# Kernel optimization log

Measured on AMD Instinct MI355X. Metric: run time of the kernel, lower is better.

The kernel has to match this reference:

```python
import jax, jax.numpy as jnp
import numpy as np

DIMS = 1024
STATE = 2 * DIMS
EPS = 1e-8


def _rmsnorm(v, scale):
    # norm = ||v||_2 * d^{-1/2}
    d = v.shape[-1]
    n = jnp.sqrt(jnp.sum(v * v, axis=-1, keepdims=True)) * (d ** -0.5)
    return scale * v / (n + EPS)


def setup_inputs() -> dict:
    key = jax.random.key(0)
    ks = jax.random.split(key, 5)
    x = jax.random.normal(ks[0], (4, 2048, DIMS), dtype=jnp.float32)
    ls_scale = jnp.ones((DIMS // 2,), dtype=jnp.float32)
    rs_scale = jnp.ones((DIMS // 2,), dtype=jnp.float32)
    split_scale = jnp.full((DIMS,), 0.1, dtype=jnp.float32)
    sk = (1.0 / DIMS) ** 0.5
    Wk = jax.random.uniform(ks[1], (DIMS, STATE), jnp.float32, -sk, sk)
    Wugg = jax.random.uniform(ks[2], (DIMS, 3 * STATE), jnp.float32, -sk, sk)
    so = (1.0 / STATE) ** 0.5
    Wout = jax.random.uniform(ks[3], (STATE, DIMS), jnp.float32, -so, so)
    return {"x": x, "ls_scale": ls_scale, "rs_scale": rs_scale,
            "split_scale": split_scale, "Wk": Wk, "Wugg": Wugg, "Wout": Wout}


def reference(x, ls_scale, rs_scale, split_scale, Wk, Wugg, Wout):
    residual = x
    # RMS_split norm (output_dim=None)
    xl, xr = jnp.split(x, 2, axis=-1)
    xn = jnp.concatenate([_rmsnorm(xl, ls_scale), _rmsnorm(xr, rs_scale)], axis=-1)
    xn = xn * split_scale

    K = jax.nn.sigmoid(xn @ Wk)                      # [B,S,STATE]
    u, g_in, g_out = jnp.split(xn @ Wugg, 3, axis=-1)
    u = u * jax.nn.sigmoid(g_in) * (1.0 - K)

    # linear recurrence: h_0 = u_0; h_t = K_{t-1} * h_{t-1} + u_t
    a = jnp.concatenate([jnp.ones_like(K[..., :1, :]), K[..., :-1, :]], axis=-2)

    def combine(lhs, rhs):
        aL, bL = lhs
        aR, bR = rhs
        return (aL * aR, bL * aR + bR)

    _, h = jax.lax.associative_scan(combine, (a, u), axis=1)
    outputs = h * jax.nn.sigmoid(g_out)
    y = outputs @ Wout
    return y + residual
```

## Files before the change

### kernel.cpp

```cpp
#include <hip/hip_runtime.h>
#include <hip/hip_bf16.h>
#include <stdint.h>

#define DIMS 1024
#define STATE 2048
#define BATCH 4
#define SEQ 2048
#define TOKENS 8192
#define N1 8192
#define NCHUNK 16
#define CHUNKL (SEQ / NCHUNK)

typedef __hip_bfloat16 bf16;
typedef __attribute__((ext_vector_type(8))) short bf16x8;
typedef __attribute__((ext_vector_type(4))) float f32x4;
typedef __attribute__((ext_vector_type(16))) float f32x16;

__device__ __forceinline__ float sigmoidf_(float x) {
  return 1.0f / (1.0f + __expf(-x));
}

__device__ __forceinline__ void async_copy16(const void* g, void* l) {
  __builtin_amdgcn_global_load_lds(
      (const __attribute__((address_space(1))) void*)(uintptr_t)g,
      (__attribute__((address_space(3))) void*)(uint32_t)(uintptr_t)l,
      16, 0, 0);
}

__device__ __forceinline__ int swz32(int row, int kc) {
  int line = row >> 1;
  int sub = ((row & 1) << 2) | kc;
  return (line << 3) | (sub ^ (line & 7));
}
__device__ __forceinline__ void swz32_dec(int c, int& row, int& kc) {
  int line = c >> 3;
  int sub = (c & 7) ^ (line & 7);
  row = (line << 1) | (sub >> 2);
  kc = sub & 3;
}
__device__ __forceinline__ int swz64(int row, int kc) {
  return (row << 3) | (kc ^ (row & 7));
}
__device__ __forceinline__ void swz64_dec(int c, int& row, int& kc) {
  row = c >> 3;
  kc = (c & 7) ^ (row & 7);
}

__global__ __launch_bounds__(256) void transpose_bf16_kernel(
    const float* __restrict__ W, bf16* __restrict__ Wt, int K, int N) {
  __shared__ float tile[32][33];
  int tx = threadIdx.x & 31;
  int ty = threadIdx.x >> 5;
  long col = (long)blockIdx.x * 32 + tx;
  long rowb = (long)blockIdx.y * 32;
#pragma unroll
  for (int i = 0; i < 32; i += 8)
    tile[ty + i][tx] = W[(rowb + ty + i) * N + col];
  __syncthreads();
  long ocol = rowb + tx;
  long orow = (long)blockIdx.x * 32 + ty;
#pragma unroll
  for (int i = 0; i < 32; i += 8)
    Wt[(orow + i) * K + ocol] = __float2bfloat16(tile[tx][ty + i]);
}

__global__ __launch_bounds__(256) void rmsnorm_kernel(
    const float* __restrict__ x, const float* __restrict__ ls,
    const float* __restrict__ rs, const float* __restrict__ ss,
    bf16* __restrict__ xn) {
  int token = blockIdx.x;
  int tid = threadIdx.x;
  const float4* xt = (const float4*)(x + (long)token * DIMS);
  float4 v = xt[tid];
  float s = v.x * v.x + v.y * v.y + v.z * v.z + v.w * v.w;
#pragma unroll
  for (int d = 32; d > 0; d >>= 1) s += __shfl_down(s, d);
  __shared__ float parts[4];
  if ((tid & 63) == 0) parts[tid >> 6] = s;
  __syncthreads();
  int j = tid * 4;
  bool left = j < 512;
  float sum = left ? (parts[0] + parts[1]) : (parts[2] + parts[3]);
  float n = sqrtf(sum * (1.0f / 512.0f));
  float inv = 1.0f / (n + 1e-8f);
  const float4* sc = (const float4*)(left ? ls : rs);
  float4 g = sc[left ? tid : tid - 128];
  float4 p = ((const float4*)ss)[tid];
  bf16* o = xn + (long)token * DIMS + j;
  o[0] = __float2bfloat16(v.x * g.x * inv * p.x);
  o[1] = __float2bfloat16(v.y * g.y * inv * p.y);
  o[2] = __float2bfloat16(v.z * g.z * inv * p.z);
  o[3] = __float2bfloat16(v.w * g.w * inv * p.w);
}

__device__ __forceinline__ void g1_stage(const bf16* __restrict__ A,
                                         const bf16* __restrict__ Bt,
                                         long arow0, long brow0, int k0,
                                         int wave, int lane, bf16* As, bf16* Bs) {
  const int K = DIMS;
#pragma unroll
  for (int i = 0; i < 4; i++) {
    int c = (wave * 4 + i) * 64 + lane;
    int row, kc; swz32_dec(c, row, kc);
    async_copy16(A + (arow0 + row) * K + k0 + kc * 8, (char*)As + (wave * 4 + i) * 1024);
  }
#pragma unroll
  for (int i = 0; i < 2; i++) {
    int c = (wave * 2 + i) * 64 + lane;
    int row, kc; swz32_dec(c, row, kc);
    async_copy16(Bt + (brow0 + row) * K + k0 + kc * 8, (char*)Bs + (wave * 2 + i) * 1024);
  }
}

__global__ __launch_bounds__(256, 2) void gemm1_big(
    const bf16* __restrict__ A, const bf16* __restrict__ Bt, bf16* __restrict__ C) {
  __shared__ __align__(16) bf16 As0[256 * 32], As1[256 * 32];
  __shared__ __align__(16) bf16 Bs0[128 * 32], Bs1[128 * 32];
  int tid = threadIdx.x;
  int lane = tid & 63, wave = tid >> 6;
  int wm = wave & 1, wn = wave >> 1;
  long arow0 = (long)blockIdx.y * 256;
  long brow0 = (long)blockIdx.x * 128;
  int m_lane = lane & 31, q4 = lane >> 5;
  f32x16 acc[4][2] = {};

  g1_stage(A, Bt, arow0, brow0, 0, wave, lane, As0, Bs0);
  __syncthreads();

  for (int it = 0; it < 32; it += 2) {
    {
      const bf16x8* AsV = (const bf16x8*)As0;
      const bf16x8* BsV = (const bf16x8*)Bs0;
      bf16x8 af[2][4], bfr[2][2];
#pragma unroll
      for (int ks = 0; ks < 2; ks++) {
        int kc = ks * 2 + q4;
#pragma unroll
        for (int mt = 0; mt < 4; mt++) af[ks][mt] = AsV[swz32(wm * 128 + mt * 32 + m_lane, kc)];
#pragma unroll
        for (int nt = 0; nt < 2; nt++) bfr[ks][nt] = BsV[swz32(wn * 64 + nt * 32 + m_lane, kc)];
      }
      g1_stage(A, Bt, arow0, brow0, (it + 1) * 32, wave, lane, As1, Bs1);
#pragma unroll
      for (int ks = 0; ks < 2; ks++)
#pragma unroll
        for (int mt = 0; mt < 4; mt++)
#pragma unroll
          for (int nt = 0; nt < 2; nt++)
            acc[mt][nt] = __builtin_amdgcn_mfma_f32_32x32x16_bf16(bfr[ks][nt], af[ks][mt], acc[mt][nt], 0, 0, 0);
      __syncthreads();
    }
    {
      const bf16x8* AsV = (const bf16x8*)As1;
      const bf16x8* BsV = (const bf16x8*)Bs1;
      bf16x8 af[2][4], bfr[2][2];
#pragma unroll
      for (int ks = 0; ks < 2; ks++) {
        int kc = ks * 2 + q4;
#pragma unroll
        for (int mt = 0; mt < 4; mt++) af[ks][mt] = AsV[swz32(wm * 128 + mt * 32 + m_lane, kc)];
#pragma unroll
        for (int nt = 0; nt < 2; nt++) bfr[ks][nt] = BsV[swz32(wn * 64 + nt * 32 + m_lane, kc)];
      }
      if (it + 2 < 32)
        g1_stage(A, Bt, arow0, brow0, (it + 2) * 32, wave, lane, As0, Bs0);
#pragma unroll
      for (int ks = 0; ks < 2; ks++)
#pragma unroll
        for (int mt = 0; mt < 4; mt++)
#pragma unroll
          for (int nt = 0; nt < 2; nt++)
            acc[mt][nt] = __builtin_amdgcn_mfma_f32_32x32x16_bf16(bfr[ks][nt], af[ks][mt], acc[mt][nt], 0, 0, 0);
      __syncthreads();
    }
  }
#pragma unroll
  for (int mt = 0; mt < 4; mt++) {
    long row = arow0 + wm * 128 + mt * 32 + m_lane;
#pragma unroll
    for (int nt = 0; nt < 2; nt++) {
#pragma unroll
      for (int g = 0; g < 4; g++) {
        long col = brow0 + wn * 64 + nt * 32 + g * 8 + q4 * 4;
        bf16 tmp[4];
#pragma unroll
        for (int j = 0; j < 4; j++) tmp[j] = __float2bfloat16(acc[mt][nt][g * 4 + j]);
        *(uint2*)(C + row * N1 + col) = *(uint2*)tmp;
      }
    }
  }
}

__device__ __forceinline__ void g2_stage(const bf16* __restrict__ A,
                                         const bf16* __restrict__ Bt,
                                         long arow0, long brow0, int k0, int K,
                                         int wave, int lane, bf16* As, bf16* Bs) {
#pragma unroll
  for (int i = 0; i < 4; i++) {
    int c = (wave * 4 + i) * 64 + lane;
    int row, kc; swz64_dec(c, row, kc);
    async_copy16(A + (arow0 + row) * K + k0 + kc * 8, (char*)As + (wave * 4 + i) * 1024);
    async_copy16(Bt + (brow0 + row) * K + k0 + kc * 8, (char*)Bs + (wave * 4 + i) * 1024);
  }
}

__global__ __launch_bounds__(256) void gemm2_resid(
    const bf16* __restrict__ A, const bf16* __restrict__ Bt,
    float* __restrict__ C, const float* __restrict__ resid) {
  __shared__ __align__(16) bf16 As0[128 * 64], As1[128 * 64];
  __shared__ __align__(16) bf16 Bs0[128 * 64], Bs1[128 * 64];
  const int K = STATE, N = DIMS;
  int tid = threadIdx.x;
  int lane = tid & 63, wave = tid >> 6;
  int wm = wave & 1, wn = wave >> 1;
  long arow0 = (long)blockIdx.y * 128;
  long brow0 = (long)blockIdx.x * 128;
  int r = lane & 15, q = lane >> 4;
  f32x4 acc[4][4] = {};

  g2_stage(A, Bt, arow0, brow0, 0, K, wave, lane, As0, Bs0);
  __syncthreads();

  for (int it = 0; it < 32; it += 2) {
    {
      const bf16x8* AsV = (const bf16x8*)As0;
      const bf16x8* BsV = (const bf16x8*)Bs0;
      bf16x8 af[2][4], bfr[2][4];
#pragma unroll
      for (int ks = 0; ks < 2; ks++) {
#pragma unroll
        for (int mt = 0; mt < 4; mt++) af[ks][mt] = AsV[swz64(wm * 64 + mt * 16 + r, ks * 4 + q)];
#pragma unroll
        for (int nt = 0; nt < 4; nt++) bfr[ks][nt] = BsV[swz64(wn * 64 + nt * 16 + r, ks * 4 + q)];
      }
      g2_stage(A, Bt, arow0, brow0, (it + 1) * 64, K, wave, lane, As1, Bs1);
#pragma unroll
      for (int ks = 0; ks < 2; ks++)
#pragma unroll
        for (int mt = 0; mt < 4; mt++)
#pragma unroll
          for (int nt = 0; nt < 4; nt++)
            acc[mt][nt] = __builtin_amdgcn_mfma_f32_16x16x32_bf16(bfr[ks][nt], af[ks][mt], acc[mt][nt], 0, 0, 0);
      __syncthreads();
    }
    {
      const bf16x8* AsV = (const bf16x8*)As1;
      const bf16x8* BsV = (const bf16x8*)Bs1;
      bf16x8 af[2][4], bfr[2][4];
#pragma unroll
      for (int ks = 0; ks < 2; ks++) {
#pragma unroll
        for (int mt = 0; mt < 4; mt++) af[ks][mt] = AsV[swz64(wm * 64 + mt * 16 + r, ks * 4 + q)];
#pragma unroll
        for (int nt = 0; nt < 4; nt++) bfr[ks][nt] = BsV[swz64(wn * 64 + nt * 16 + r, ks * 4 + q)];
      }
      if (it + 2 < 32)
        g2_stage(A, Bt, arow0, brow0, (it + 2) * 64, K, wave, lane, As0, Bs0);
#pragma unroll
      for (int ks = 0; ks < 2; ks++)
#pragma unroll
        for (int mt = 0; mt < 4; mt++)
#pragma unroll
          for (int nt = 0; nt < 4; nt++)
            acc[mt][nt] = __builtin_amdgcn_mfma_f32_16x16x32_bf16(bfr[ks][nt], af[ks][mt], acc[mt][nt], 0, 0, 0);
      __syncthreads();
    }
  }

#pragma unroll
  for (int mt = 0; mt < 4; mt++) {
    long row = arow0 + wm * 64 + mt * 16 + r;
#pragma unroll
    for (int nt = 0; nt < 4; nt++) {
      long col = brow0 + wn * 64 + nt * 16 + q * 4;
      float4 rv = *(const float4*)(resid + row * N + col);
      float4 ov;
      ov.x = acc[mt][nt][0] + rv.x;
      ov.y = acc[mt][nt][1] + rv.y;
      ov.z = acc[mt][nt][2] + rv.z;
      ov.w = acc[mt][nt][3] + rv.w;
      *(float4*)(C + row * N + col) = ov;
    }
  }
}


__global__ __launch_bounds__(256) void chunk_summary_kernel(
    const bf16* __restrict__ C1, float* __restrict__ carryA,
    float* __restrict__ carryU) {
  int b = blockIdx.x;
  int ch = blockIdx.y * 256 + threadIdx.x;
  int chunk = blockIdx.z;
  int t0 = chunk * CHUNKL;
  long base = ((long)b * SEQ) * N1 + ch;
  float kp = 0.0f;
  if (chunk != 0) kp = __bfloat162float(C1[base + (long)(t0 - 1) * N1]);
  float a_first = (chunk == 0) ? 1.0f : sigmoidf_(kp);
  float A = 1.0f, U = 0.0f;
#pragma unroll 8
  for (int t = t0; t < t0 + CHUNKL; t++) {
    long off = base + (long)t * N1;
    float kraw = __bfloat162float(C1[off]);
    float uraw = __bfloat162float(C1[off + 2048]);
    float gin  = __bfloat162float(C1[off + 4096]);
    float a = (t == t0) ? a_first : sigmoidf_(kp);
    float sK = sigmoidf_(kraw);
    float u = uraw * sigmoidf_(gin) * (1.0f - sK);
    A *= a;
    U = a * U + u;
    kp = kraw;
  }
  int cidx = (b * NCHUNK + chunk) * STATE + ch;
  carryA[cidx] = A;
  carryU[cidx] = U;
}

__global__ __launch_bounds__(256) void carry_scan_kernel(
    const float* __restrict__ carryA, const float* __restrict__ carryU,
    float* __restrict__ carryIn) {
  int idx = blockIdx.x * 256 + threadIdx.x;
  int b = idx >> 11;
  int ch = idx & 2047;
  float h = 0.0f;
#pragma unroll
  for (int c = 0; c < NCHUNK; c++) {
    int cidx = (b * NCHUNK + c) * STATE + ch;
    carryIn[cidx] = h;
    h = carryA[cidx] * h + carryU[cidx];
  }
}

__global__ __launch_bounds__(256) void scan_chunk_kernel(
    const bf16* __restrict__ C1, const float* __restrict__ carryIn,
    bf16* __restrict__ out) {
  int b = blockIdx.x;
  int c0 = blockIdx.y * 32;
  int chunk = blockIdx.z;
  int tstart = chunk * CHUNKL;
  __shared__ float a_s[32][65], u_s[32][65], h_s[32][65];
  int tid = threadIdx.x;
  int lane = tid & 63, wave = tid >> 6;
  int cc = tid & 31;
  int tq = tid >> 5;

  float carryH[8], carryK[8];
#pragma unroll
  for (int i = 0; i < 8; i++) {
    int ch = c0 + wave * 8 + i;
    carryH[i] = carryIn[(b * NCHUNK + chunk) * STATE + ch];
    carryK[i] = (chunk == 0)
                    ? 1.0f
                    : sigmoidf_(__bfloat162float(
                          C1[((long)(b * SEQ + tstart - 1)) * N1 + ch]));
  }

  float g_r[8];
  for (int t0 = tstart; t0 < tstart + CHUNKL; t0 += 64) {
#pragma unroll
    for (int i = 0; i < 8; i++) {
      int t = tq * 8 + i;
      long rowoff = ((long)(b * SEQ + t0 + t)) * N1 + c0 + cc;
      float kraw = __bfloat162float(C1[rowoff]);
      float uraw = __bfloat162float(C1[rowoff + 2048]);
      float gin  = __bfloat162float(C1[rowoff + 4096]);
      float gout = __bfloat162float(C1[rowoff + 6144]);
      float aK = sigmoidf_(kraw);
      a_s[cc][t] = aK;
      u_s[cc][t] = uraw * sigmoidf_(gin) * (1.0f - aK);
      g_r[i] = sigmoidf_(gout);
    }
    __syncthreads();
#pragma unroll
    for (int i = 0; i < 8; i++) {
      int ch = wave * 8 + i;
      float aK = a_s[ch][lane];
      float u = u_s[ch][lane];
      float a = __shfl_up(aK, 1);
      if (lane == 0) a = carryK[i];
      float A = a, U = u;
#pragma unroll
      for (int d = 1; d < 64; d <<= 1) {
        float Au = __shfl_up(A, d);
        float Uu = __shfl_up(U, d);
        if (lane >= d) { U += A * Uu; A *= Au; }
      }
      float h = U + A * carryH[i];
      carryH[i] = __shfl(h, 63);
      carryK[i] = __shfl(aK, 63);
      h_s[ch][lane] = h;
    }
    __syncthreads();
#pragma unroll
    for (int i = 0; i < 8; i++) {
      int t = tq * 8 + i;
      out[((long)(b * SEQ + t0 + t)) * STATE + c0 + cc] =
          __float2bfloat16(h_s[cc][t] * g_r[i]);
    }
    __syncthreads();
  }
}

extern "C" void kernel_launch(void* const* d_in, const int* in_sizes, int n_in,
                              void* d_out, int out_size, void* d_ws, size_t ws_size,
                              hipStream_t stream) {
  const float* x    = (const float*)d_in[0];
  const float* ls   = (const float*)d_in[1];
  const float* rs   = (const float*)d_in[2];
  const float* ss   = (const float*)d_in[3];
  const float* Wk   = (const float*)d_in[4];
  const float* Wugg = (const float*)d_in[5];
  const float* Wout = (const float*)d_in[6];
  float* out = (float*)d_out;

  char* ws = (char*)d_ws;
  bf16* W1t = (bf16*)ws;
  bf16* W2t = (bf16*)(ws + 16777216);
  bf16* xn  = (bf16*)(ws + 16777216 + 4194304);
  bf16* C1  = (bf16*)(ws + 16777216 + 4194304 + 16777216);
  bf16* sco = (bf16*)(ws + 16777216 + 4194304 + 16777216 + 134217728);
  float* carryA  = (float*)xn;
  float* carryU  = carryA + BATCH * NCHUNK * STATE;
  float* carryIn = carryU + BATCH * NCHUNK * STATE;

  transpose_bf16_kernel<<<dim3(STATE / 32, DIMS / 32), 256, 0, stream>>>(Wk, W1t, DIMS, STATE);
  transpose_bf16_kernel<<<dim3(3 * STATE / 32, DIMS / 32), 256, 0, stream>>>(
      Wugg, W1t + (long)STATE * DIMS, DIMS, 3 * STATE);
  transpose_bf16_kernel<<<dim3(DIMS / 32, STATE / 32), 256, 0, stream>>>(Wout, W2t, STATE, DIMS);

  rmsnorm_kernel<<<TOKENS, 256, 0, stream>>>(x, ls, rs, ss, xn);

  gemm1_big<<<dim3(N1 / 128, TOKENS / 256), 256, 0, stream>>>(xn, W1t, C1);

  chunk_summary_kernel<<<dim3(BATCH, STATE / 256, NCHUNK), 256, 0, stream>>>(
      C1, carryA, carryU);
  carry_scan_kernel<<<dim3(BATCH * STATE / 256), 256, 0, stream>>>(
      carryA, carryU, carryIn);
  scan_chunk_kernel<<<dim3(BATCH, STATE / 32, NCHUNK), 256, 0, stream>>>(
      C1, carryIn, sco);

  gemm2_resid<<<dim3(DIMS / 128, TOKENS / 128), 256, 0, stream>>>(
      sco, W2t, out, x);
}
```

Baseline: 444.8 us.

## Run the first projection GEMM in FP8 with static scaling

Quantizes the normalized activations and the Wk/Wugg weights to FP8 e4m3 with fixed power-of-two scales, and runs the first large GEMM with FP8 MFMA instructions. The K dimension is permuted so that each 16-byte LDS load feeds two MFMAs. The goal is to halve the memory traffic and LDS footprint per K step and to use the higher FP8 matrix throughput. The cost is lower precision in the gate and input projections, which may not meet the accuracy tolerance.

After: 404.8 us. 1.1x faster.

```diff
diff --git a/kernel.cpp b/kernel.cpp
--- a/kernel.cpp
+++ b/kernel.cpp
@@ -1,5 +1,6 @@
 #include <hip/hip_runtime.h>
 #include <hip/hip_bf16.h>
+#include <hip/hip_fp8.h>
 #include <stdint.h>
 
 #define DIMS 1024
@@ -12,12 +13,27 @@
 #define CHUNKL (SEQ / NCHUNK)
 
 typedef __hip_bfloat16 bf16;
+typedef unsigned char u8;
 typedef __attribute__((ext_vector_type(8))) short bf16x8;
 typedef __attribute__((ext_vector_type(4))) float f32x4;
 typedef __attribute__((ext_vector_type(16))) float f32x16;
+typedef __attribute__((ext_vector_type(2))) long v2i64;
+
+#define XN_SCALE 32.0f
+#define W1_SCALE 256.0f
+#define INV_SCALE (1.0f / 8192.0f)
 
 __device__ __forceinline__ float sigmoidf_(float x) {
   return 1.0f / (1.0f + __expf(-x));
+}
+
+__device__ __forceinline__ u8 to_fp8(float f) {
+  __hip_fp8_e4m3 h(f);
+  return h.__x;
+}
+
+__device__ __forceinline__ int kperm(int k) {
+  return (k & ~24) | ((k & 8) << 1) | ((k & 16) >> 1);
 }
 
 __device__ __forceinline__ void async_copy16(const void* g, void* l) {
@@ -64,10 +80,28 @@
     Wt[(orow + i) * K + ocol] = __float2bfloat16(tile[tx][ty + i]);
 }
 
+__global__ __launch_bounds__(256) void transpose_fp8_kernel(
+    const float* __restrict__ W, u8* __restrict__ Wt, int K, int N) {
+  __shared__ float tile[32][33];
+  int tx = threadIdx.x & 31;
+  int ty = threadIdx.x >> 5;
+  long col = (long)blockIdx.x * 32 + tx;
+  long rowb = (long)blockIdx.y * 32;
+#pragma unroll
+  for (int i = 0; i < 32; i += 8)
+    tile[ty + i][tx] = W[(rowb + ty + i) * N + col];
+  __syncthreads();
+  long ocol = rowb + kperm(tx);
+  long orow = (long)blockIdx.x * 32 + ty;
+#pragma unroll
+  for (int i = 0; i < 32; i += 8)
+    Wt[(orow + i) * K + ocol] = to_fp8(tile[tx][ty + i] * W1_SCALE);
+}
+
 __global__ __launch_bounds__(256) void rmsnorm_kernel(
     const float* __restrict__ x, const float* __restrict__ ls,
     const float* __restrict__ rs, const float* __restrict__ ss,
-    bf16* __restrict__ xn) {
+    u8* __restrict__ xn8) {
   int token = blockIdx.x;
   int tid = threadIdx.x;
   const float4* xt = (const float4*)(x + (long)token * DIMS);
@@ -86,36 +120,37 @@
   const float4* sc = (const float4*)(left ? ls : rs);
   float4 g = sc[left ? tid : tid - 128];
   float4 p = ((const float4*)ss)[tid];
-  bf16* o = xn + (long)token * DIMS + j;
-  o[0] = __float2bfloat16(v.x * g.x * inv * p.x);
-  o[1] = __float2bfloat16(v.y * g.y * inv * p.y);
-  o[2] = __float2bfloat16(v.z * g.z * inv * p.z);
-  o[3] = __float2bfloat16(v.w * g.w * inv * p.w);
-}
-
-__device__ __forceinline__ void g1_stage(const bf16* __restrict__ A,
-                                         const bf16* __restrict__ Bt,
-                                         long arow0, long brow0, int k0,
-                                         int wave, int lane, bf16* As, bf16* Bs) {
+  u8 q[4];
+  q[0] = to_fp8(v.x * g.x * inv * p.x * XN_SCALE);
+  q[1] = to_fp8(v.y * g.y * inv * p.y * XN_SCALE);
+  q[2] = to_fp8(v.z * g.z * inv * p.z * XN_SCALE);
+  q[3] = to_fp8(v.w * g.w * inv * p.w * XN_SCALE);
+  *(uint32_t*)(xn8 + (long)token * DIMS + kperm(j)) = *(uint32_t*)q;
+}
+
+__device__ __forceinline__ void g1f8_stage(const u8* __restrict__ A,
+                                           const u8* __restrict__ Bt,
+                                           long arow0, long brow0, int k0,
+                                           int wave, int lane, u8* As, u8* Bs) {
   const int K = DIMS;
 #pragma unroll
   for (int i = 0; i < 4; i++) {
     int c = (wave * 4 + i) * 64 + lane;
     int row, kc; swz32_dec(c, row, kc);
-    async_copy16(A + (arow0 + row) * K + k0 + kc * 8, (char*)As + (wave * 4 + i) * 1024);
+    async_copy16(A + (arow0 + row) * K + k0 + kc * 16, (char*)As + (wave * 4 + i) * 1024);
   }
 #pragma unroll
   for (int i = 0; i < 2; i++) {
     int c = (wave * 2 + i) * 64 + lane;
     int row, kc; swz32_dec(c, row, kc);
-    async_copy16(Bt + (brow0 + row) * K + k0 + kc * 8, (char*)Bs + (wave * 2 + i) * 1024);
-  }
-}
-
-__global__ __launch_bounds__(256, 2) void gemm1_big(
-    const bf16* __restrict__ A, const bf16* __restrict__ Bt, bf16* __restrict__ C) {
-  __shared__ __align__(16) bf16 As0[256 * 32], As1[256 * 32];
-  __shared__ __align__(16) bf16 Bs0[128 * 32], Bs1[128 * 32];
+    async_copy16(Bt + (brow0 + row) * K + k0 + kc * 16, (char*)Bs + (wave * 2 + i) * 1024);
+  }
+}
+
+__global__ __launch_bounds__(256, 2) void gemm1_fp8(
+    const u8* __restrict__ A, const u8* __restrict__ Bt, bf16* __restrict__ C) {
+  __shared__ __align__(16) u8 As0[256 * 64], As1[256 * 64];
+  __shared__ __align__(16) u8 Bs0[128 * 64], Bs1[128 * 64];
   int tid = threadIdx.x;
   int lane = tid & 63, wave = tid >> 6;
   int wm = wave & 1, wn = wave >> 1;
@@ -124,53 +159,55 @@
   int m_lane = lane & 31, q4 = lane >> 5;
   f32x16 acc[4][2] = {};
 
-  g1_stage(A, Bt, arow0, brow0, 0, wave, lane, As0, Bs0);
+  g1f8_stage(A, Bt, arow0, brow0, 0, wave, lane, As0, Bs0);
   __syncthreads();
 
-  for (int it = 0; it < 32; it += 2) {
+  for (int it = 0; it < 16; it += 2) {
     {
-      const bf16x8* AsV = (const bf16x8*)As0;
-      const bf16x8* BsV = (const bf16x8*)Bs0;
-      bf16x8 af[2][4], bfr[2][2];
-#pragma unroll
-      for (int ks = 0; ks < 2; ks++) {
-        int kc = ks * 2 + q4;
-#pragma unroll
-        for (int mt = 0; mt < 4; mt++) af[ks][mt] = AsV[swz32(wm * 128 + mt * 32 + m_lane, kc)];
-#pragma unroll
-        for (int nt = 0; nt < 2; nt++) bfr[ks][nt] = BsV[swz32(wn * 64 + nt * 32 + m_lane, kc)];
-      }
-      g1_stage(A, Bt, arow0, brow0, (it + 1) * 32, wave, lane, As1, Bs1);
-#pragma unroll
-      for (int ks = 0; ks < 2; ks++)
-#pragma unroll
-        for (int mt = 0; mt < 4; mt++)
-#pragma unroll
-          for (int nt = 0; nt < 2; nt++)
-            acc[mt][nt] = __builtin_amdgcn_mfma_f32_32x32x16_bf16(bfr[ks][nt], af[ks][mt], acc[mt][nt], 0, 0, 0);
+      v2i64 af[2][4], bfr[2][2];
+#pragma unroll
+      for (int p = 0; p < 2; p++) {
+#pragma unroll
+        for (int mt = 0; mt < 4; mt++)
+          af[p][mt] = *(const v2i64*)(As0 + swz32(wm * 128 + mt * 32 + m_lane, p * 2 + q4) * 16);
+#pragma unroll
+        for (int nt = 0; nt < 2; nt++)
+          bfr[p][nt] = *(const v2i64*)(Bs0 + swz32(wn * 64 + nt * 32 + m_lane, p * 2 + q4) * 16);
+      }
+      g1f8_stage(A, Bt, arow0, brow0, (it + 1) * 64, wave, lane, As1, Bs1);
+#pragma unroll
+      for (int p = 0; p < 2; p++)
+#pragma unroll
+        for (int mt = 0; mt < 4; mt++)
+#pragma unroll
+          for (int nt = 0; nt < 2; nt++) {
+            acc[mt][nt] = __builtin_amdgcn_mfma_f32_32x32x16_fp8_fp8(bfr[p][nt][0], af[p][mt][0], acc[mt][nt], 0, 0, 0);
+            acc[mt][nt] = __builtin_amdgcn_mfma_f32_32x32x16_fp8_fp8(bfr[p][nt][1], af[p][mt][1], acc[mt][nt], 0, 0, 0);
+          }
       __syncthreads();
     }
     {
-      const bf16x8* AsV = (const bf16x8*)As1;
-      const bf16x8* BsV = (const bf16x8*)Bs1;
-      bf16x8 af[2][4], bfr[2][2];
-#pragma unroll
-      for (int ks = 0; ks < 2; ks++) {
-        int kc = ks * 2 + q4;
-#pragma unroll
-        for (int mt = 0; mt < 4; mt++) af[ks][mt] = AsV[swz32(wm * 128 + mt * 32 + m_lane, kc)];
-#pragma unroll
-        for (int nt = 0; nt < 2; nt++) bfr[ks][nt] = BsV[swz32(wn * 64 + nt * 32 + m_lane, kc)];
-      }
-      if (it + 2 < 32)
-        g1_stage(A, Bt, arow0, brow0, (it + 2) * 32, wave, lane, As0, Bs0);
-#pragma unroll
-      for (int ks = 0; ks < 2; ks++)
-#pragma unroll
-        for (int mt = 0; mt < 4; mt++)
-#pragma unroll
-          for (int nt = 0; nt < 2; nt++)
-            acc[mt][nt] = __builtin_amdgcn_mfma_f32_32x32x16_bf16(bfr[ks][nt], af[ks][mt], acc[mt][nt], 0, 0, 0);
+      v2i64 af[2][4], bfr[2][2];
+#pragma unroll
+      for (int p = 0; p < 2; p++) {
+#pragma unroll
+        for (int mt = 0; mt < 4; mt++)
+          af[p][mt] = *(const v2i64*)(As1 + swz32(wm * 128 + mt * 32 + m_lane, p * 2 + q4) * 16);
+#pragma unroll
+        for (int nt = 0; nt < 2; nt++)
+          bfr[p][nt] = *(const v2i64*)(Bs1 + swz32(wn * 64 + nt * 32 + m_lane, p * 2 + q4) * 16);
+      }
+      if (it + 2 < 16)
+        g1f8_stage(A, Bt, arow0, brow0, (it + 2) * 64, wave, lane, As0, Bs0);
+#pragma unroll
+      for (int p = 0; p < 2; p++)
+#pragma unroll
+        for (int mt = 0; mt < 4; mt++)
+#pragma unroll
+          for (int nt = 0; nt < 2; nt++) {
+            acc[mt][nt] = __builtin_amdgcn_mfma_f32_32x32x16_fp8_fp8(bfr[p][nt][0], af[p][mt][0], acc[mt][nt], 0, 0, 0);
+            acc[mt][nt] = __builtin_amdgcn_mfma_f32_32x32x16_fp8_fp8(bfr[p][nt][1], af[p][mt][1], acc[mt][nt], 0, 0, 0);
+          }
       __syncthreads();
     }
   }
@@ -184,7 +221,8 @@
         long col = brow0 + wn * 64 + nt * 32 + g * 8 + q4 * 4;
         bf16 tmp[4];
 #pragma unroll
-        for (int j = 0; j < 4; j++) tmp[j] = __float2bfloat16(acc[mt][nt][g * 4 + j]);
+        for (int j = 0; j < 4; j++)
+          tmp[j] = __float2bfloat16(acc[mt][nt][g * 4 + j] * INV_SCALE);
         *(uint2*)(C + row * N1 + col) = *(uint2*)tmp;
       }
     }
@@ -413,23 +451,23 @@
   float* out = (float*)d_out;
 
   char* ws = (char*)d_ws;
-  bf16* W1t = (bf16*)ws;
-  bf16* W2t = (bf16*)(ws + 16777216);
-  bf16* xn  = (bf16*)(ws + 16777216 + 4194304);
-  bf16* C1  = (bf16*)(ws + 16777216 + 4194304 + 16777216);
-  bf16* sco = (bf16*)(ws + 16777216 + 4194304 + 16777216 + 134217728);
-  float* carryA  = (float*)xn;
+  u8*   W1f8 = (u8*)ws;
+  bf16* W2t  = (bf16*)(ws + 8388608);
+  u8*   xn8  = (u8*)(ws + 8388608 + 4194304);
+  bf16* C1   = (bf16*)(ws + 8388608 + 4194304 + 8388608);
+  bf16* sco  = (bf16*)(ws + 8388608 + 4194304 + 8388608 + 134217728);
+  float* carryA  = (float*)xn8;
   float* carryU  = carryA + BATCH * NCHUNK * STATE;
   float* carryIn = carryU + BATCH * NCHUNK * STATE;
 
-  transpose_bf16_kernel<<<dim3(STATE / 32, DIMS / 32), 256, 0, stream>>>(Wk, W1t, DIMS, STATE);
-  transpose_bf16_kernel<<<dim3(3 * STATE / 32, DIMS / 32), 256, 0, stream>>>(
-      Wugg, W1t + (long)STATE * DIMS, DIMS, 3 * STATE);
+  transpose_fp8_kernel<<<dim3(STATE / 32, DIMS / 32), 256, 0, stream>>>(Wk, W1f8, DIMS, STATE);
+  transpose_fp8_kernel<<<dim3(3 * STATE / 32, DIMS / 32), 256, 0, stream>>>(
+      Wugg, W1f8 + (long)STATE * DIMS, DIMS, 3 * STATE);
   transpose_bf16_kernel<<<dim3(DIMS / 32, STATE / 32), 256, 0, stream>>>(Wout, W2t, STATE, DIMS);
 
-  rmsnorm_kernel<<<TOKENS, 256, 0, stream>>>(x, ls, rs, ss, xn);
-
-  gemm1_big<<<dim3(N1 / 128, TOKENS / 256), 256, 0, stream>>>(xn, W1t, C1);
+  rmsnorm_kernel<<<TOKENS, 256, 0, stream>>>(x, ls, rs, ss, xn8);
+
+  gemm1_fp8<<<dim3(N1 / 128, TOKENS / 256), 256, 0, stream>>>(xn8, W1f8, C1);
 
   chunk_summary_kernel<<<dim3(BATCH, STATE / 256, NCHUNK), 256, 0, stream>>>(
       C1, carryA, carryU);
```
